# Kernel tuning notes

Hardware: AMD Instinct MI355X
Metric: run time of the kernel (lower is better)

## Reference

```python
import jax, jax.numpy as jnp
import numpy as np

INNER_STEPS = 50
INNER_LR = 0.1
Y_MEAN = 0.0


def _mlp(params, inp):
    # eqx.nn.MLP(in=3, out=1, width=64, depth=3): relu hidden, identity final
    W1, b1, W2, b2, W3, b3, W4, b4 = params
    h = jax.nn.relu(W1 @ inp + b1)
    h = jax.nn.relu(W2 @ h + b2)
    h = jax.nn.relu(W3 @ h + b3)
    return jnp.squeeze(W4 @ h + b4)


def setup_inputs() -> dict:
    key = jax.random.key(0)
    ks = jax.random.split(key, 10)
    B, CD, W = 8192, 1, 64
    d_in = 2 + CD
    x = jax.random.normal(ks[0], (B, 1), dtype=jnp.float32)
    c = jax.random.normal(ks[1], (B, CD), dtype=jnp.float32)
    def lin(k, fan_out, fan_in):
        lim = 1.0 / np.sqrt(fan_in)
        kw, kb = jax.random.split(k)
        Wm = jax.random.uniform(kw, (fan_out, fan_in), minval=-lim, maxval=lim, dtype=jnp.float32)
        bm = jax.random.uniform(kb, (fan_out,), minval=-lim, maxval=lim, dtype=jnp.float32)
        return Wm, bm
    W1, b1 = lin(ks[2], W, d_in)
    W2, b2 = lin(ks[3], W, W)
    W3, b3 = lin(ks[4], W, W)
    W4, b4 = lin(ks[5], 1, W)
    return {"x": x, "c": c, "W1": W1, "b1": b1, "W2": W2, "b2": b2,
            "W3": W3, "b3": b3, "W4": W4, "b4": b4}


def reference(x, c, W1, b1, W2, b2, W3, b3, W4, b4):
    params = (W1, b1, W2, b2, W3, b3, W4, b4)
    # nearest-neighbor c0 per sample (excluding self)
    dists = jnp.linalg.norm(c[:, None, :] - c[None, :, :], axis=-1)  # [B,B]
    dists = dists + jnp.eye(dists.shape[0], dtype=dists.dtype) * 1e9
    c0 = c[jnp.argmin(dists, axis=1)]  # [B,CD]

    def base_energy(xi, yi, ci):
        return _mlp(params, jnp.concatenate([xi, yi, ci], axis=0))

    def solve(xi, ci, c0i):
        y0 = jnp.array([Y_MEAN], dtype=xi.dtype)

        def step(y, _):
            def loss(yy):
                E0, dE = jax.jvp(lambda cc: base_energy(xi, yy, cc), (c0i,), (ci - c0i,))
                return E0 + dE
            gy = jax.grad(loss)(y)
            return y - INNER_LR * gy, None

        yf, _ = jax.lax.scan(step, y0, None, length=INNER_STEPS)
        return yf

    return jax.vmap(solve)(x, c, c0)  # [B,1]
```

## Files before the change

kernel.cpp:

```cpp
#include <hip/hip_runtime.h>

#define BATCH 8192
#define LOSC  2048.0f
#define LOINV (1.0f / 2048.0f)

typedef _Float16 f16x4 __attribute__((ext_vector_type(4)));
typedef __fp16   fp16x2 __attribute__((ext_vector_type(2)));
typedef float    f32x4 __attribute__((ext_vector_type(4)));

union PK2 { fp16x2 h; unsigned u; };
union U4  { f16x4 v; unsigned u[2]; };

__device__ __forceinline__ unsigned pkrtz(float a, float b) {
    PK2 p; p.h = __builtin_amdgcn_cvt_pkrtz(a, b); return p.u;
}
__device__ __forceinline__ float lo0(unsigned hp, float v) {
    PK2 p; p.u = hp; return (v - (float)p.h[0]) * LOSC;
}
__device__ __forceinline__ float lo1(unsigned hp, float v) {
    PK2 p; p.u = hp; return (v - (float)p.h[1]) * LOSC;
}

__global__ __launch_bounds__(256) void nn_kernel(const float* __restrict__ c,
                                                 float* __restrict__ c0) {
    __shared__ float cs[BATCH];
    const int t = threadIdx.x;
    {
        const float4* cg = (const float4*)c;
        float4* cl = (float4*)cs;
        for (int j = t; j < BATCH / 4; j += 256) cl[j] = cg[j];
    }
    __syncthreads();
    const int part = t & 31;
    const int i    = blockIdx.x * 8 + (t >> 5);
    const float ci = cs[i];
    const int sj0 = ((i & 3) == 0) ? (i >> 2) : -1;
    const int sj1 = ((i & 3) == 1) ? (i >> 2) : -1;
    const int sj2 = ((i & 3) == 2) ? (i >> 2) : -1;
    const int sj3 = ((i & 3) == 3) ? (i >> 2) : -1;
    const float4* cs4 = (const float4*)cs;
    float bd0 = 3e38f, bd1 = 3e38f, bd2 = 3e38f, bd3 = 3e38f;
    int   bj0 = 0,     bj1 = 0,     bj2 = 0,     bj3 = 0;
    #pragma unroll 4
    for (int tt = 0; tt < 64; ++tt) {
        const int jj = part + (tt << 5);
        const float4 v = cs4[jj];
        float d0 = fabsf(ci - v.x);
        float d1 = fabsf(ci - v.y);
        float d2 = fabsf(ci - v.z);
        float d3 = fabsf(ci - v.w);
        if (jj == sj0) d0 = 3e38f;
        if (jj == sj1) d1 = 3e38f;
        if (jj == sj2) d2 = 3e38f;
        if (jj == sj3) d3 = 3e38f;
        if (d0 < bd0) { bd0 = d0; bj0 = jj; }
        if (d1 < bd1) { bd1 = d1; bj1 = jj; }
        if (d2 < bd2) { bd2 = d2; bj2 = jj; }
        if (d3 < bd3) { bd3 = d3; bj3 = jj; }
    }
    float best = bd0; int bestj = bj0 * 4 + 0;
    { const int j1 = bj1 * 4 + 1; if (bd1 < best || (bd1 == best && j1 < bestj)) { best = bd1; bestj = j1; } }
    { const int j2 = bj2 * 4 + 2; if (bd2 < best || (bd2 == best && j2 < bestj)) { best = bd2; bestj = j2; } }
    { const int j3 = bj3 * 4 + 3; if (bd3 < best || (bd3 == best && j3 < bestj)) { best = bd3; bestj = j3; } }
    #pragma unroll
    for (int off = 1; off < 32; off <<= 1) {
        const float od = __shfl_xor(best, off);
        const int   oj = __shfl_xor(bestj, off);
        if (od < best || (od == best && oj < bestj)) { best = od; bestj = oj; }
    }
    if (part == 0) c0[i] = cs[bestj];
}

__global__ __launch_bounds__(64, 1) void solve_kernel(
    const float* __restrict__ x, const float* __restrict__ c0g,
    const float* __restrict__ W1, const float* __restrict__ b1,
    const float* __restrict__ W2, const float* __restrict__ b2,
    const float* __restrict__ W3, const float* __restrict__ b3,
    const float* __restrict__ W4, float* __restrict__ out)
{
    const int lane = threadIdx.x & 63;
    const int q  = lane >> 4;
    const int cc = lane & 15;
    const bool fwd = (cc < 8);
    const int s = cc & 7;
    const int sbase = blockIdx.x * 8;

    f16x4 W2h[4][4], W2l[4][4], W3h[4][4], W3l[4][4];
    #pragma unroll
    for (int T = 0; T < 4; ++T)
        #pragma unroll
        for (int m = 0; m < 4; ++m) {
            const int off = (T * 16 + cc) * 64 + m * 16 + q * 4;
            const float4 w2 = *(const float4*)(W2 + off);
            const float4 w3 = *(const float4*)(W3 + off);
            U4 h, l;
            h.u[0] = pkrtz(w2.x, w2.y); h.u[1] = pkrtz(w2.z, w2.w);
            l.u[0] = pkrtz(lo0(h.u[0], w2.x), lo1(h.u[0], w2.y));
            l.u[1] = pkrtz(lo0(h.u[1], w2.z), lo1(h.u[1], w2.w));
            W2h[T][m] = h.v; W2l[T][m] = l.v;
            h.u[0] = pkrtz(w3.x, w3.y); h.u[1] = pkrtz(w3.z, w3.w);
            l.u[0] = pkrtz(lo0(h.u[0], w3.x), lo1(h.u[0], w3.y));
            l.u[1] = pkrtz(lo0(h.u[1], w3.z), lo1(h.u[1], w3.w));
            W3h[T][m] = h.v; W3l[T][m] = l.v;
        }

    float b2m[16], b3m[16], w4r[16];
    #pragma unroll
    for (int T = 0; T < 4; ++T)
        #pragma unroll
        for (int r = 0; r < 4; ++r) {
            const int row = T * 16 + q * 4 + r;
            b2m[T * 4 + r] = fwd ? b2[row] : 0.f;
            b3m[T * 4 + r] = fwd ? b3[row] : 0.f;
            w4r[T * 4 + r] = W4[row];
        }

    float A1v[16], w11v[16];
    {
        const float xs  = x[sbase + s];
        const float c0s = c0g[sbase + s];
        #pragma unroll
        for (int m = 0; m < 4; ++m)
            #pragma unroll
            for (int j = 0; j < 4; ++j) {
                const int k = m * 16 + q * 4 + j;
                w11v[m * 4 + j] = W1[k * 3 + 1];
                A1v[m * 4 + j]  = fmaf(xs, W1[k * 3 + 0],
                                       fmaf(c0s, W1[k * 3 + 2], b1[k]));
            }
    }

    float y = 0.0f;

    #pragma unroll 1
    for (int step = 0; step < 50; ++step) {
        U4 B1h[4], B1l[4];
        #pragma unroll
        for (int m = 0; m < 4; ++m) {
            float v[4];
            #pragma unroll
            for (int j = 0; j < 4; ++j) {
                const float w = w11v[m * 4 + j];
                const float z = fmaf(y, w, A1v[m * 4 + j]);
                v[j] = fwd ? fmaxf(z, 0.f) : (z > 0.f ? w : 0.f);
            }
            const unsigned h0 = pkrtz(v[0], v[1]);
            const unsigned h1 = pkrtz(v[2], v[3]);
            B1h[m].u[0] = h0; B1h[m].u[1] = h1;
            B1l[m].u[0] = pkrtz(lo0(h0, v[0]), lo1(h0, v[1]));
            B1l[m].u[1] = pkrtz(lo0(h1, v[2]), lo1(h1, v[3]));
        }
        f32x4 ZH[4], ZL[4];
        #pragma unroll
        for (int T = 0; T < 4; ++T) {
            f32x4 aH;
            aH[0] = b2m[T * 4 + 0]; aH[1] = b2m[T * 4 + 1];
            aH[2] = b2m[T * 4 + 2]; aH[3] = b2m[T * 4 + 3];
            f32x4 aL = {0.f, 0.f, 0.f, 0.f};
            #pragma unroll
            for (int m = 0; m < 4; ++m) {
                aH = __builtin_amdgcn_mfma_f32_16x16x16f16(W2h[T][m], B1h[m].v, aH, 0, 0, 0);
                aL = __builtin_amdgcn_mfma_f32_16x16x16f16(W2h[T][m], B1l[m].v, aL, 0, 0, 0);
                aL = __builtin_amdgcn_mfma_f32_16x16x16f16(W2l[T][m], B1h[m].v, aL, 0, 0, 0);
            }
            ZH[T] = aH; ZL[T] = aL;
        }
        U4 B2h[4], B2l[4];
        #pragma unroll
        for (int T = 0; T < 4; ++T) {
            float v[4];
            #pragma unroll
            for (int r = 0; r < 4; ++r) {
                const float z = fmaf(ZL[T][r], LOINV, ZH[T][r]);
                const float recv = __shfl_xor(z, 8);
                v[r] = fwd ? fmaxf(z, 0.f) : (recv > 0.f ? z : 0.f);
            }
            const unsigned h0 = pkrtz(v[0], v[1]);
            const unsigned h1 = pkrtz(v[2], v[3]);
            B2h[T].u[0] = h0; B2h[T].u[1] = h1;
            B2l[T].u[0] = pkrtz(lo0(h0, v[0]), lo1(h0, v[1]));
            B2l[T].u[1] = pkrtz(lo0(h1, v[2]), lo1(h1, v[3]));
        }
        #pragma unroll
        for (int T = 0; T < 4; ++T) {
            f32x4 aH;
            aH[0] = b3m[T * 4 + 0]; aH[1] = b3m[T * 4 + 1];
            aH[2] = b3m[T * 4 + 2]; aH[3] = b3m[T * 4 + 3];
            f32x4 aL = {0.f, 0.f, 0.f, 0.f};
            #pragma unroll
            for (int m = 0; m < 4; ++m) {
                aH = __builtin_amdgcn_mfma_f32_16x16x16f16(W3h[T][m], B2h[m].v, aH, 0, 0, 0);
                aL = __builtin_amdgcn_mfma_f32_16x16x16f16(W3h[T][m], B2l[m].v, aL, 0, 0, 0);
                aL = __builtin_amdgcn_mfma_f32_16x16x16f16(W3l[T][m], B2h[m].v, aL, 0, 0, 0);
            }
            ZH[T] = aH; ZL[T] = aL;
        }
        float g = 0.f;
        #pragma unroll
        for (int T = 0; T < 4; ++T)
            #pragma unroll
            for (int r = 0; r < 4; ++r) {
                const float z = fmaf(ZL[T][r], LOINV, ZH[T][r]);
                const float recv  = __shfl_xor(z, 8);
                const float maskv = fwd ? z : recv;
                const float valv  = fwd ? recv : z;
                g = fmaf(w4r[T * 4 + r], (maskv > 0.f) ? valv : 0.f, g);
            }
        g += __shfl_xor(g, 16);
        g += __shfl_xor(g, 32);
        y -= 0.1f * g;
    }
    if (lane < 8) out[sbase + lane] = y;
}

extern "C" void kernel_launch(void* const* d_in, const int* in_sizes, int n_in,
                              void* d_out, int out_size, void* d_ws, size_t ws_size,
                              hipStream_t stream) {
    const float* x  = (const float*)d_in[0];
    const float* c  = (const float*)d_in[1];
    const float* W1 = (const float*)d_in[2];
    const float* b1 = (const float*)d_in[3];
    const float* W2 = (const float*)d_in[4];
    const float* b2 = (const float*)d_in[5];
    const float* W3 = (const float*)d_in[6];
    const float* b3 = (const float*)d_in[7];
    const float* W4 = (const float*)d_in[8];
    float* c0  = (float*)d_ws;
    float* out = (float*)d_out;

    nn_kernel<<<BATCH / 8, 256, 0, stream>>>(c, c0);
    solve_kernel<<<BATCH / 8, 64, 0, stream>>>(x, c0, W1, b1, W2, b2, W3, b3, W4, out);
}
```

Measured before the change: 169.5 us.

## Fuse nearest-neighbor search into solve kernel and use 16x16x32 MFMA

Drops the separate nearest-neighbor kernel. Each 64-lane solve block now loads all of c into LDS and finds the neighbors of its 8 samples itself, 8 lanes per sample, before the inner optimisation loop. This removes a launch and the workspace round-trip, but each block now does a 32KB LDS fill and a longer serial scan with fewer threads. Separately, the MFMA path moves from 16x16x16 to 16x16x32 f16 instructions with 8-wide fragments, halving the MFMA instruction count per layer.

```diff
diff --git a/kernel.cpp b/kernel.cpp
--- a/kernel.cpp
+++ b/kernel.cpp
@@ -4,12 +4,12 @@
 #define LOSC  2048.0f
 #define LOINV (1.0f / 2048.0f)
 
-typedef _Float16 f16x4 __attribute__((ext_vector_type(4)));
+typedef _Float16 f16x8 __attribute__((ext_vector_type(8)));
 typedef __fp16   fp16x2 __attribute__((ext_vector_type(2)));
 typedef float    f32x4 __attribute__((ext_vector_type(4)));
 
 union PK2 { fp16x2 h; unsigned u; };
-union U4  { f16x4 v; unsigned u[2]; };
+union U8  { f16x8 v; unsigned u[4]; };
 
 __device__ __forceinline__ unsigned pkrtz(float a, float b) {
     PK2 p; p.h = __builtin_amdgcn_cvt_pkrtz(a, b); return p.u;
@@ -21,87 +21,101 @@
     PK2 p; p.u = hp; return (v - (float)p.h[1]) * LOSC;
 }
 
-__global__ __launch_bounds__(256) void nn_kernel(const float* __restrict__ c,
-                                                 float* __restrict__ c0) {
-    __shared__ float cs[BATCH];
-    const int t = threadIdx.x;
-    {
-        const float4* cg = (const float4*)c;
-        float4* cl = (float4*)cs;
-        for (int j = t; j < BATCH / 4; j += 256) cl[j] = cg[j];
-    }
-    __syncthreads();
-    const int part = t & 31;
-    const int i    = blockIdx.x * 8 + (t >> 5);
-    const float ci = cs[i];
-    const int sj0 = ((i & 3) == 0) ? (i >> 2) : -1;
-    const int sj1 = ((i & 3) == 1) ? (i >> 2) : -1;
-    const int sj2 = ((i & 3) == 2) ? (i >> 2) : -1;
-    const int sj3 = ((i & 3) == 3) ? (i >> 2) : -1;
-    const float4* cs4 = (const float4*)cs;
-    float bd0 = 3e38f, bd1 = 3e38f, bd2 = 3e38f, bd3 = 3e38f;
-    int   bj0 = 0,     bj1 = 0,     bj2 = 0,     bj3 = 0;
-    #pragma unroll 4
-    for (int tt = 0; tt < 64; ++tt) {
-        const int jj = part + (tt << 5);
-        const float4 v = cs4[jj];
-        float d0 = fabsf(ci - v.x);
-        float d1 = fabsf(ci - v.y);
-        float d2 = fabsf(ci - v.z);
-        float d3 = fabsf(ci - v.w);
-        if (jj == sj0) d0 = 3e38f;
-        if (jj == sj1) d1 = 3e38f;
-        if (jj == sj2) d2 = 3e38f;
-        if (jj == sj3) d3 = 3e38f;
-        if (d0 < bd0) { bd0 = d0; bj0 = jj; }
-        if (d1 < bd1) { bd1 = d1; bj1 = jj; }
-        if (d2 < bd2) { bd2 = d2; bj2 = jj; }
-        if (d3 < bd3) { bd3 = d3; bj3 = jj; }
-    }
-    float best = bd0; int bestj = bj0 * 4 + 0;
-    { const int j1 = bj1 * 4 + 1; if (bd1 < best || (bd1 == best && j1 < bestj)) { best = bd1; bestj = j1; } }
-    { const int j2 = bj2 * 4 + 2; if (bd2 < best || (bd2 == best && j2 < bestj)) { best = bd2; bestj = j2; } }
-    { const int j3 = bj3 * 4 + 3; if (bd3 < best || (bd3 == best && j3 < bestj)) { best = bd3; bestj = j3; } }
-    #pragma unroll
-    for (int off = 1; off < 32; off <<= 1) {
-        const float od = __shfl_xor(best, off);
-        const int   oj = __shfl_xor(bestj, off);
-        if (od < best || (od == best && oj < bestj)) { best = od; bestj = oj; }
-    }
-    if (part == 0) c0[i] = cs[bestj];
-}
-
 __global__ __launch_bounds__(64, 1) void solve_kernel(
-    const float* __restrict__ x, const float* __restrict__ c0g,
+    const float* __restrict__ x, const float* __restrict__ c,
     const float* __restrict__ W1, const float* __restrict__ b1,
     const float* __restrict__ W2, const float* __restrict__ b2,
     const float* __restrict__ W3, const float* __restrict__ b3,
     const float* __restrict__ W4, float* __restrict__ out)
 {
-    const int lane = threadIdx.x & 63;
+    const int lane  = threadIdx.x & 63;
+    const int sbase = blockIdx.x * 8;
+
+    __shared__ float cs[BATCH];
+    {
+        const float4* cg = (const float4*)c;
+        float4* cl = (float4*)cs;
+        #pragma unroll
+        for (int j = 0; j < BATCH / 4 / 64; ++j)
+            cl[lane + j * 64] = cg[lane + j * 64];
+    }
+    __syncthreads();
+
+    float c0s;
+    {
+        const int g  = lane >> 3;
+        const int p  = lane & 7;
+        const int si = sbase + g;
+        const float ci = cs[si];
+        const int sj0 = ((si & 3) == 0) ? (si >> 2) : -1;
+        const int sj1 = ((si & 3) == 1) ? (si >> 2) : -1;
+        const int sj2 = ((si & 3) == 2) ? (si >> 2) : -1;
+        const int sj3 = ((si & 3) == 3) ? (si >> 2) : -1;
+        const float4* cs4 = (const float4*)cs;
+        float bd0 = 3e38f, bd1 = 3e38f, bd2 = 3e38f, bd3 = 3e38f;
+        int   bj0 = 0,     bj1 = 0,     bj2 = 0,     bj3 = 0;
+        #pragma unroll 4
+        for (int tt = 0; tt < 256; ++tt) {
+            const int jj = p + (tt << 3);
+            const float4 v = cs4[jj];
+            float d0 = fabsf(ci - v.x);
+            float d1 = fabsf(ci - v.y);
+            float d2 = fabsf(ci - v.z);
+            float d3 = fabsf(ci - v.w);
+            if (jj == sj0) d0 = 3e38f;
+            if (jj == sj1) d1 = 3e38f;
+            if (jj == sj2) d2 = 3e38f;
+            if (jj == sj3) d3 = 3e38f;
+            if (d0 < bd0) { bd0 = d0; bj0 = jj; }
+            if (d1 < bd1) { bd1 = d1; bj1 = jj; }
+            if (d2 < bd2) { bd2 = d2; bj2 = jj; }
+            if (d3 < bd3) { bd3 = d3; bj3 = jj; }
+        }
+        float best = bd0; int bestj = bj0 * 4 + 0;
+        { const int j1 = bj1 * 4 + 1; if (bd1 < best || (bd1 == best && j1 < bestj)) { best = bd1; bestj = j1; } }
+        { const int j2 = bj2 * 4 + 2; if (bd2 < best || (bd2 == best && j2 < bestj)) { best = bd2; bestj = j2; } }
+        { const int j3 = bj3 * 4 + 3; if (bd3 < best || (bd3 == best && j3 < bestj)) { best = bd3; bestj = j3; } }
+        #pragma unroll
+        for (int off = 1; off < 8; off <<= 1) {
+            const float od = __shfl_xor(best, off);
+            const int   oj = __shfl_xor(bestj, off);
+            if (od < best || (od == best && oj < bestj)) { best = od; bestj = oj; }
+        }
+        const float bestc = cs[bestj];
+        c0s = __shfl(bestc, (lane & 7) << 3);
+    }
+
     const int q  = lane >> 4;
     const int cc = lane & 15;
     const bool fwd = (cc < 8);
     const int s = cc & 7;
-    const int sbase = blockIdx.x * 8;
-
-    f16x4 W2h[4][4], W2l[4][4], W3h[4][4], W3l[4][4];
+
+    f16x8 W2h[4][2], W2l[4][2], W3h[4][2], W3l[4][2];
     #pragma unroll
     for (int T = 0; T < 4; ++T)
         #pragma unroll
-        for (int m = 0; m < 4; ++m) {
-            const int off = (T * 16 + cc) * 64 + m * 16 + q * 4;
-            const float4 w2 = *(const float4*)(W2 + off);
-            const float4 w3 = *(const float4*)(W3 + off);
-            U4 h, l;
-            h.u[0] = pkrtz(w2.x, w2.y); h.u[1] = pkrtz(w2.z, w2.w);
-            l.u[0] = pkrtz(lo0(h.u[0], w2.x), lo1(h.u[0], w2.y));
-            l.u[1] = pkrtz(lo0(h.u[1], w2.z), lo1(h.u[1], w2.w));
-            W2h[T][m] = h.v; W2l[T][m] = l.v;
-            h.u[0] = pkrtz(w3.x, w3.y); h.u[1] = pkrtz(w3.z, w3.w);
-            l.u[0] = pkrtz(lo0(h.u[0], w3.x), lo1(h.u[0], w3.y));
-            l.u[1] = pkrtz(lo0(h.u[1], w3.z), lo1(h.u[1], w3.w));
-            W3h[T][m] = h.v; W3l[T][m] = l.v;
+        for (int M = 0; M < 2; ++M) {
+            const int off0 = (T * 16 + cc) * 64 + M * 32 + q * 4;
+            const int off1 = off0 + 16;
+            float4 a = *(const float4*)(W2 + off0);
+            float4 b = *(const float4*)(W2 + off1);
+            U8 h, l;
+            h.u[0] = pkrtz(a.x, a.y); h.u[1] = pkrtz(a.z, a.w);
+            h.u[2] = pkrtz(b.x, b.y); h.u[3] = pkrtz(b.z, b.w);
+            l.u[0] = pkrtz(lo0(h.u[0], a.x), lo1(h.u[0], a.y));
+            l.u[1] = pkrtz(lo0(h.u[1], a.z), lo1(h.u[1], a.w));
+            l.u[2] = pkrtz(lo0(h.u[2], b.x), lo1(h.u[2], b.y));
+            l.u[3] = pkrtz(lo0(h.u[3], b.z), lo1(h.u[3], b.w));
+            W2h[T][M] = h.v; W2l[T][M] = l.v;
+            a = *(const float4*)(W3 + off0);
+            b = *(const float4*)(W3 + off1);
+            h.u[0] = pkrtz(a.x, a.y); h.u[1] = pkrtz(a.z, a.w);
+            h.u[2] = pkrtz(b.x, b.y); h.u[3] = pkrtz(b.z, b.w);
+            l.u[0] = pkrtz(lo0(h.u[0], a.x), lo1(h.u[0], a.y));
+            l.u[1] = pkrtz(lo0(h.u[1], a.z), lo1(h.u[1], a.w));
+            l.u[2] = pkrtz(lo0(h.u[2], b.x), lo1(h.u[2], b.y));
+            l.u[3] = pkrtz(lo0(h.u[3], b.z), lo1(h.u[3], b.w));
+            W3h[T][M] = h.v; W3l[T][M] = l.v;
         }
 
     float b2m[16], b3m[16], w4r[16];
@@ -117,8 +131,7 @@
 
     float A1v[16], w11v[16];
     {
-        const float xs  = x[sbase + s];
-        const float c0s = c0g[sbase + s];
+        const float xs = x[sbase + s];
         #pragma unroll
         for (int m = 0; m < 4; ++m)
             #pragma unroll
@@ -134,7 +147,7 @@
 
     #pragma unroll 1
     for (int step = 0; step < 50; ++step) {
-        U4 B1h[4], B1l[4];
+        U8 B1h[2], B1l[2];
         #pragma unroll
         for (int m = 0; m < 4; ++m) {
             float v[4];
@@ -146,9 +159,11 @@
             }
             const unsigned h0 = pkrtz(v[0], v[1]);
             const unsigned h1 = pkrtz(v[2], v[3]);
-            B1h[m].u[0] = h0; B1h[m].u[1] = h1;
-            B1l[m].u[0] = pkrtz(lo0(h0, v[0]), lo1(h0, v[1]));
-            B1l[m].u[1] = pkrtz(lo0(h1, v[2]), lo1(h1, v[3]));
+            const int M = m >> 1, o = (m & 1) * 2;
+            B1h[M].u[o]     = h0;
+            B1h[M].u[o + 1] = h1;
+            B1l[M].u[o]     = pkrtz(lo0(h0, v[0]), lo1(h0, v[1]));
+            B1l[M].u[o + 1] = pkrtz(lo0(h1, v[2]), lo1(h1, v[3]));
         }
         f32x4 ZH[4], ZL[4];
         #pragma unroll
@@ -158,14 +173,14 @@
             aH[2] = b2m[T * 4 + 2]; aH[3] = b2m[T * 4 + 3];
             f32x4 aL = {0.f, 0.f, 0.f, 0.f};
             #pragma unroll
-            for (int m = 0; m < 4; ++m) {
-                aH = __builtin_amdgcn_mfma_f32_16x16x16f16(W2h[T][m], B1h[m].v, aH, 0, 0, 0);
-                aL = __builtin_amdgcn_mfma_f32_16x16x16f16(W2h[T][m], B1l[m].v, aL, 0, 0, 0);
-                aL = __builtin_amdgcn_mfma_f32_16x16x16f16(W2l[T][m], B1h[m].v, aL, 0, 0, 0);
+            for (int M = 0; M < 2; ++M) {
+                aH = __builtin_amdgcn_mfma_f32_16x16x32_f16(W2h[T][M], B1h[M].v, aH, 0, 0, 0);
+                aL = __builtin_amdgcn_mfma_f32_16x16x32_f16(W2h[T][M], B1l[M].v, aL, 0, 0, 0);
+                aL = __builtin_amdgcn_mfma_f32_16x16x32_f16(W2l[T][M], B1h[M].v, aL, 0, 0, 0);
             }
             ZH[T] = aH; ZL[T] = aL;
         }
-        U4 B2h[4], B2l[4];
+        U8 B2h[2], B2l[2];
         #pragma unroll
         for (int T = 0; T < 4; ++T) {
             float v[4];
@@ -177,9 +192,11 @@
             }
             const unsigned h0 = pkrtz(v[0], v[1]);
             const unsigned h1 = pkrtz(v[2], v[3]);
-            B2h[T].u[0] = h0; B2h[T].u[1] = h1;
-            B2l[T].u[0] = pkrtz(lo0(h0, v[0]), lo1(h0, v[1]));
-            B2l[T].u[1] = pkrtz(lo0(h1, v[2]), lo1(h1, v[3]));
+            const int M = T >> 1, o = (T & 1) * 2;
+            B2h[M].u[o]     = h0;
+            B2h[M].u[o + 1] = h1;
+            B2l[M].u[o]     = pkrtz(lo0(h0, v[0]), lo1(h0, v[1]));
+            B2l[M].u[o + 1] = pkrtz(lo0(h1, v[2]), lo1(h1, v[3]));
         }
         #pragma unroll
         for (int T = 0; T < 4; ++T) {
@@ -188,10 +205,10 @@
             aH[2] = b3m[T * 4 + 2]; aH[3] = b3m[T * 4 + 3];
             f32x4 aL = {0.f, 0.f, 0.f, 0.f};
             #pragma unroll
-            for (int m = 0; m < 4; ++m) {
-                aH = __builtin_amdgcn_mfma_f32_16x16x16f16(W3h[T][m], B2h[m].v, aH, 0, 0, 0);
-                aL = __builtin_amdgcn_mfma_f32_16x16x16f16(W3h[T][m], B2l[m].v, aL, 0, 0, 0);
-                aL = __builtin_amdgcn_mfma_f32_16x16x16f16(W3l[T][m], B2h[m].v, aL, 0, 0, 0);
+            for (int M = 0; M < 2; ++M) {
+                aH = __builtin_amdgcn_mfma_f32_16x16x32_f16(W3h[T][M], B2h[M].v, aH, 0, 0, 0);
+                aL = __builtin_amdgcn_mfma_f32_16x16x32_f16(W3h[T][M], B2l[M].v, aL, 0, 0, 0);
+                aL = __builtin_amdgcn_mfma_f32_16x16x32_f16(W3l[T][M], B2h[M].v, aL, 0, 0, 0);
             }
             ZH[T] = aH; ZL[T] = aL;
         }
@@ -225,9 +242,7 @@
     const float* W3 = (const float*)d_in[6];
     const float* b3 = (const float*)d_in[7];
     const float* W4 = (const float*)d_in[8];
-    float* c0  = (float*)d_ws;
     float* out = (float*)d_out;
 
-    nn_kernel<<<BATCH / 8, 256, 0, stream>>>(c, c0);
-    solve_kernel<<<BATCH / 8, 64, 0, stream>>>(x, c0, W1, b1, W2, b2, W3, b3, W4, out);
-}
+    solve_kernel<<<BATCH / 8, 64, 0, stream>>>(x, c, W1, b1, W2, b2, W3, b3, W4, out);
+}
```

Result: no change. 167.2 us (-1.4%).
